# Kernel tuning notes

Measured on AMD Instinct MI355X. Metric: run time of the kernel, lower is better.

The kernel has to match this reference:

```python
import jax, jax.numpy as jnp
import numpy as np

NEG_SLOPE = 0.2
BN_EPS = 1e-5


def _gatv2(x, src, dst, Wl, Wr, att, b, N, concat):
    # x: [N, Cin]; src/dst: [E] (self-loops already appended)
    H, F = att.shape
    xl = (x @ Wl).reshape(N, H, F)  # source transform
    xr = (x @ Wr).reshape(N, H, F)  # target transform
    s = jax.nn.leaky_relu(xl[src] + xr[dst], NEG_SLOPE)  # [E,H,F]
    e = jnp.einsum('ehf,hf->eh', s, att)                  # [E,H]
    m = jax.ops.segment_max(e, dst, num_segments=N)       # [N,H]
    ex = jnp.exp(e - m[dst])
    den = jax.ops.segment_sum(ex, dst, num_segments=N)
    alpha = ex / den[dst]                                 # [E,H] softmax over in-edges
    out = jax.ops.segment_sum(alpha[:, :, None] * xl[src], dst, num_segments=N)  # [N,H,F]
    out = out.reshape(N, H * F) if concat else out.mean(axis=1)
    return out + b


def _bn_eval(x, g, b, rm, rv):
    return (x - rm) * jax.lax.rsqrt(rv + BN_EPS) * g + b


def setup_inputs() -> dict:
    key = jax.random.key(0)
    ks = jax.random.split(key, 16)
    N, E, Cin, Fh, H, Cout = 50000, 800000, 128, 64, 4, 128
    Hm = H * Fh  # 256
    d = {
        'x': jax.random.normal(ks[0], (N, Cin), jnp.float32),
        'edge_index': jax.random.randint(ks[1], (2, E), 0, N, jnp.int64),
        'Wl1': jax.random.normal(ks[2], (Cin, Hm), jnp.float32) / np.sqrt(Cin),
        'Wr1': jax.random.normal(ks[3], (Cin, Hm), jnp.float32) / np.sqrt(Cin),
        'att1': jax.random.normal(ks[4], (H, Fh), jnp.float32) / np.sqrt(Fh),
        'b1': jnp.zeros((Hm,), jnp.float32),
        'bn1_g': jax.random.uniform(ks[5], (Hm,), jnp.float32, 0.5, 1.5),
        'bn1_b': 0.1 * jax.random.normal(ks[6], (Hm,), jnp.float32),
        'bn1_m': jnp.zeros((Hm,), jnp.float32),
        'bn1_v': jnp.ones((Hm,), jnp.float32),
        'Wl2': jax.random.normal(ks[7], (Hm, Hm), jnp.float32) / np.sqrt(Hm),
        'Wr2': jax.random.normal(ks[8], (Hm, Hm), jnp.float32) / np.sqrt(Hm),
        'att2': jax.random.normal(ks[9], (H, Fh), jnp.float32) / np.sqrt(Fh),
        'b2': jnp.zeros((Hm,), jnp.float32),
        'bn2_g': jax.random.uniform(ks[10], (Hm,), jnp.float32, 0.5, 1.5),
        'bn2_b': 0.1 * jax.random.normal(ks[11], (Hm,), jnp.float32),
        'bn2_m': jnp.zeros((Hm,), jnp.float32),
        'bn2_v': jnp.ones((Hm,), jnp.float32),
        'Wl3': jax.random.normal(ks[12], (Hm, Cout), jnp.float32) / np.sqrt(Hm),
        'Wr3': jax.random.normal(ks[13], (Hm, Cout), jnp.float32) / np.sqrt(Hm),
        'att3': jax.random.normal(ks[14], (1, Cout), jnp.float32) / np.sqrt(Cout),
        'b3': jnp.zeros((Cout,), jnp.float32),
    }
    return d


def reference(x, edge_index, Wl1, Wr1, att1, b1, bn1_g, bn1_b, bn1_m, bn1_v,
              Wl2, Wr2, att2, b2, bn2_g, bn2_b, bn2_m, bn2_v,
              Wl3, Wr3, att3, b3):
    N = x.shape[0]
    loop = jnp.arange(N, dtype=edge_index.dtype)
    src = jnp.concatenate([edge_index[0], loop])  # add self-loops (PyG default)
    dst = jnp.concatenate([edge_index[1], loop])
    h = _gatv2(x, src, dst, Wl1, Wr1, att1, b1, N, True)
    h = jax.nn.elu(_bn_eval(h, bn1_g, bn1_b, bn1_m, bn1_v))  # dropout=identity (eval)
    h = _gatv2(h, src, dst, Wl2, Wr2, att2, b2, N, True)
    h = jax.nn.elu(_bn_eval(h, bn2_g, bn2_b, bn2_m, bn2_v))
    return _gatv2(h, src, dst, Wl3, Wr3, att3, b3, N, False)
```

## Files before the change

### kernel.cpp

```cpp
#include <hip/hip_runtime.h>
#include <math.h>

#define NEG_SLOPE 0.2f
#define BN_EPS 1e-5f

typedef _Float16 f16x8 __attribute__((ext_vector_type(8)));
typedef float f32x4 __attribute__((ext_vector_type(4)));

__device__ __forceinline__ void async_copy16(const void* g, void* l) {
  __builtin_amdgcn_global_load_lds(
      (const __attribute__((address_space(1))) void*)g,
      (__attribute__((address_space(3))) void*)l, 16, 0, 0);
}

__device__ __forceinline__ float2 unpack2(unsigned int u) {
  union { unsigned int u; _Float16 h[2]; } c; c.u = u;
  return make_float2((float)c.h[0], (float)c.h[1]);
}
__device__ __forceinline__ unsigned int pack2(float a, float b) {
  union { unsigned int u; _Float16 h[2]; } c;
  c.h[0] = (_Float16)a; c.h[1] = (_Float16)b; return c.u;
}
__device__ __forceinline__ float4 unpack4(uint2 u) {
  union { uint2 u2; _Float16 h[4]; } c; c.u2 = u;
  return make_float4((float)c.h[0], (float)c.h[1], (float)c.h[2], (float)c.h[3]);
}
__device__ __forceinline__ uint2 pack4(float4 v) {
  union { uint2 u2; _Float16 h[4]; } c;
  c.h[0] = (_Float16)v.x; c.h[1] = (_Float16)v.y;
  c.h[2] = (_Float16)v.z; c.h[3] = (_Float16)v.w;
  return c.u2;
}

__global__ void k_zero_i32(int* __restrict__ p, int n) {
  int i = blockIdx.x * blockDim.x + threadIdx.x;
  if (i < n) p[i] = 0;
}

__global__ void k_f2h(const float* __restrict__ in, unsigned int* __restrict__ out, int n2) {
  int i = blockIdx.x * blockDim.x + threadIdx.x;
  if (i < n2) {
    float2 v = reinterpret_cast<const float2*>(in)[i];
    out[i] = pack2(v.x, v.y);
  }
}

__global__ void k_prep_w(const float* __restrict__ Wl, const float* __restrict__ Wr,
                         int K, int Ch, _Float16* __restrict__ WT) {
  int i = blockIdx.x * blockDim.x + threadIdx.x;
  int total = 2 * Ch * K;
  if (i >= total) return;
  int c = i / K, k = i % K;
  float v = (c < Ch) ? Wl[(size_t)k * Ch + c] : Wr[(size_t)k * Ch + (c - Ch)];
  WT[i] = (_Float16)v;
}

__global__ void k_count(const int* __restrict__ ei, int E, int N, int* __restrict__ deg) {
  int e = blockIdx.x * blockDim.x + threadIdx.x;
  int T = E + N;
  if (e >= T) return;
  int d = (e < E) ? ei[E + e] : (e - E);
  atomicAdd(&deg[d], 1);
}

__global__ __launch_bounds__(1024) void k_scan(const int* __restrict__ deg, int N,
                                               int* __restrict__ offs, int* __restrict__ cursor) {
  __shared__ int wsum[16];
  __shared__ int s_base;
  int t = threadIdx.x;
  int lane = t & 63, w = t >> 6;
  if (t == 0) s_base = 0;
  __syncthreads();
  for (int start = 0; start < N; start += 1024) {
    int i = start + t;
    int v = (i < N) ? deg[i] : 0;
    int val = v;
    #pragma unroll
    for (int off = 1; off < 64; off <<= 1) {
      int x = __shfl_up(val, off, 64);
      if (lane >= off) val += x;
    }
    if (lane == 63) wsum[w] = val;
    __syncthreads();
    if (w == 0) {
      int s = (lane < 16) ? wsum[lane] : 0;
      #pragma unroll
      for (int off = 1; off < 16; off <<= 1) {
        int x = __shfl_up(s, off, 64);
        if (lane >= off) s += x;
      }
      if (lane < 16) wsum[lane] = s;
    }
    __syncthreads();
    int base = s_base;
    int woff = (w > 0) ? wsum[w - 1] : 0;
    int excl = base + woff + (val - v);
    if (i < N) { offs[i] = excl; cursor[i] = excl; }
    int total = wsum[15];
    __syncthreads();
    if (t == 0) s_base = base + total;
    __syncthreads();
  }
  if (t == 0) offs[N] = s_base;
}

__global__ void k_scatter(const int* __restrict__ ei, int E, int N,
                          int* __restrict__ cursor, int* __restrict__ csr_src) {
  int e = blockIdx.x * blockDim.x + threadIdx.x;
  int T = E + N;
  if (e < 4) csr_src[T + e] = 0;
  if (e >= T) return;
  int s, d;
  if (e < E) { s = ei[e]; d = ei[E + e]; } else { s = d = e - E; }
  int pos = atomicAdd(&cursor[d], 1);
  csr_src[pos] = s;
}

__global__ __launch_bounds__(256) void k_hgemm(const _Float16* __restrict__ A,
                                               const _Float16* __restrict__ BT,
                                               _Float16* __restrict__ C,
                                               int M, int Ntot, int K) {
  __shared__ _Float16 As[128 * 64];
  __shared__ _Float16 Bs[128 * 64];
  const int t = threadIdx.x;
  const int lane = t & 63, w = t >> 6;
  const int wr = w >> 1, wc = w & 1;
  const int bm0 = blockIdx.x * 128, bn0 = blockIdx.y * 128;
  f32x4 acc[4][4] = {};
  const int nkt = K >> 6;
  for (int kt = 0; kt < nkt; ++kt) {
    __syncthreads();
    #pragma unroll
    for (int i = 0; i < 4; ++i) {
      int q = (i * 4 + w) * 64 + lane;
      int row = q >> 3, sl = q & 7;
      int ssrc = sl ^ (row & 7);
      int ga = bm0 + row; if (ga >= M) ga = M - 1;
      async_copy16(&A[(size_t)ga * K + kt * 64 + ssrc * 8], &As[q * 8]);
      async_copy16(&BT[(size_t)(bn0 + row) * K + kt * 64 + ssrc * 8], &Bs[q * 8]);
    }
    __syncthreads();
    #pragma unroll
    for (int ks = 0; ks < 2; ++ks) {
      f16x8 a[4], b[4];
      const int sl = ks * 4 + (lane >> 4);
      #pragma unroll
      for (int mi = 0; mi < 4; ++mi) {
        int row = wr * 64 + mi * 16 + (lane & 15);
        a[mi] = *(const f16x8*)&As[(row * 8 + (sl ^ (row & 7))) * 8];
      }
      #pragma unroll
      for (int ni = 0; ni < 4; ++ni) {
        int row = wc * 64 + ni * 16 + (lane & 15);
        b[ni] = *(const f16x8*)&Bs[(row * 8 + (sl ^ (row & 7))) * 8];
      }
      #pragma unroll
      for (int mi = 0; mi < 4; ++mi)
        #pragma unroll
        for (int ni = 0; ni < 4; ++ni)
          acc[mi][ni] = __builtin_amdgcn_mfma_f32_16x16x32_f16(a[mi], b[ni], acc[mi][ni], 0, 0, 0);
    }
  }
  const int r0 = (lane >> 4) * 4;
  const int cc = lane & 15;
  #pragma unroll
  for (int mi = 0; mi < 4; ++mi) {
    #pragma unroll
    for (int r = 0; r < 4; ++r) {
      int row = bm0 + wr * 64 + mi * 16 + r0 + r;
      if (row >= M) continue;
      #pragma unroll
      for (int ni = 0; ni < 4; ++ni) {
        int col = bn0 + wc * 64 + ni * 16 + cc;
        C[(size_t)row * Ntot + col] = (_Float16)acc[mi][ni][r];
      }
    }
  }
}

__global__ __launch_bounds__(128) void k_gat4(const _Float16* __restrict__ xlr,
                                              const float* __restrict__ att, const float* __restrict__ bias,
                                              const float* __restrict__ g, const float* __restrict__ bb,
                                              const float* __restrict__ rm, const float* __restrict__ rv,
                                              const int* __restrict__ offs, const int* __restrict__ csr,
                                              int N, _Float16* __restrict__ hout) {
  const int n = blockIdx.x * 2 + (threadIdx.x >> 6);
  if (n >= N) return;
  const int l4 = (threadIdx.x & 63);
  const uint2* xu2 = (const uint2*)xlr;
  const float4 xr4 = unpack4(xu2[(size_t)n * 128 + 64 + l4]);
  const float4 at4 = reinterpret_cast<const float4*>(att)[l4];
  const int j0 = offs[n], j1 = offs[n + 1];

  float m = -INFINITY, l = 0.f;
  float4 acc = make_float4(0.f, 0.f, 0.f, 0.f);

  int j = j0;
  int s1 = csr[j0], s2 = csr[j0 + 1];
  uint2 u1 = xu2[(size_t)s1 * 128 + l4];
  uint2 u2 = xu2[(size_t)s2 * 128 + l4];

  for (; j + 1 < j1; j += 2) {
    int s1n = csr[j + 2], s2n = csr[j + 3];
    uint2 u1n = xu2[(size_t)s1n * 128 + l4];
    uint2 u2n = xu2[(size_t)s2n * 128 + l4];

    float4 v1 = unpack4(u1), v2 = unpack4(u2);
    float t0, e1, e2;
    t0 = v1.x + xr4.x; t0 = t0 > 0.f ? t0 : NEG_SLOPE * t0; e1  = t0 * at4.x;
    t0 = v1.y + xr4.y; t0 = t0 > 0.f ? t0 : NEG_SLOPE * t0; e1 += t0 * at4.y;
    t0 = v1.z + xr4.z; t0 = t0 > 0.f ? t0 : NEG_SLOPE * t0; e1 += t0 * at4.z;
    t0 = v1.w + xr4.w; t0 = t0 > 0.f ? t0 : NEG_SLOPE * t0; e1 += t0 * at4.w;
    t0 = v2.x + xr4.x; t0 = t0 > 0.f ? t0 : NEG_SLOPE * t0; e2  = t0 * at4.x;
    t0 = v2.y + xr4.y; t0 = t0 > 0.f ? t0 : NEG_SLOPE * t0; e2 += t0 * at4.y;
    t0 = v2.z + xr4.z; t0 = t0 > 0.f ? t0 : NEG_SLOPE * t0; e2 += t0 * at4.z;
    t0 = v2.w + xr4.w; t0 = t0 > 0.f ? t0 : NEG_SLOPE * t0; e2 += t0 * at4.w;
    #pragma unroll
    for (int off = 1; off < 16; off <<= 1) {
      e1 += __shfl_xor(e1, off, 64);
      e2 += __shfl_xor(e2, off, 64);
    }
    float mn = fmaxf(m, fmaxf(e1, e2));
    float c  = __expf(m - mn);
    float p1 = __expf(e1 - mn);
    float p2 = __expf(e2 - mn);
    l = l * c + p1 + p2;
    acc.x = acc.x * c + p1 * v1.x + p2 * v2.x;
    acc.y = acc.y * c + p1 * v1.y + p2 * v2.y;
    acc.z = acc.z * c + p1 * v1.z + p2 * v2.z;
    acc.w = acc.w * c + p1 * v1.w + p2 * v2.w;
    m = mn;
    u1 = u1n; u2 = u2n;
  }
  if (j < j1) {
    float4 v1 = unpack4(u1);
    float t0, e1;
    t0 = v1.x + xr4.x; t0 = t0 > 0.f ? t0 : NEG_SLOPE * t0; e1  = t0 * at4.x;
    t0 = v1.y + xr4.y; t0 = t0 > 0.f ? t0 : NEG_SLOPE * t0; e1 += t0 * at4.y;
    t0 = v1.z + xr4.z; t0 = t0 > 0.f ? t0 : NEG_SLOPE * t0; e1 += t0 * at4.z;
    t0 = v1.w + xr4.w; t0 = t0 > 0.f ? t0 : NEG_SLOPE * t0; e1 += t0 * at4.w;
    #pragma unroll
    for (int off = 1; off < 16; off <<= 1) e1 += __shfl_xor(e1, off, 64);
    float mn = fmaxf(m, e1);
    float c  = __expf(m - mn);
    float p1 = __expf(e1 - mn);
    l = l * c + p1;
    acc.x = acc.x * c + p1 * v1.x;
    acc.y = acc.y * c + p1 * v1.y;
    acc.z = acc.z * c + p1 * v1.z;
    acc.w = acc.w * c + p1 * v1.w;
  }
  const float4 b4  = reinterpret_cast<const float4*>(bias)[l4];
  const float4 rm4 = reinterpret_cast<const float4*>(rm)[l4];
  const float4 rv4 = reinterpret_cast<const float4*>(rv)[l4];
  const float4 g4  = reinterpret_cast<const float4*>(g)[l4];
  const float4 bb4 = reinterpret_cast<const float4*>(bb)[l4];
  float inv = 1.f / l;
  float4 o;
  o.x = (acc.x * inv + b4.x - rm4.x) * rsqrtf(rv4.x + BN_EPS) * g4.x + bb4.x;
  o.y = (acc.y * inv + b4.y - rm4.y) * rsqrtf(rv4.y + BN_EPS) * g4.y + bb4.y;
  o.z = (acc.z * inv + b4.z - rm4.z) * rsqrtf(rv4.z + BN_EPS) * g4.z + bb4.z;
  o.w = (acc.w * inv + b4.w - rm4.w) * rsqrtf(rv4.w + BN_EPS) * g4.w + bb4.w;
  o.x = o.x > 0.f ? o.x : (__expf(o.x) - 1.f);
  o.y = o.y > 0.f ? o.y : (__expf(o.y) - 1.f);
  o.z = o.z > 0.f ? o.z : (__expf(o.z) - 1.f);
  o.w = o.w > 0.f ? o.w : (__expf(o.w) - 1.f);
  ((uint2*)hout)[(size_t)n * 64 + l4] = pack4(o);
}

__global__ __launch_bounds__(128) void k_gat1(const _Float16* __restrict__ xlr,
                                              const float* __restrict__ att, const float* __restrict__ bias,
                                              const int* __restrict__ offs, const int* __restrict__ csr,
                                              int N, float* __restrict__ out) {
  const int n = blockIdx.x * 2 + (threadIdx.x >> 6);
  if (n >= N) return;
  const int l2 = (threadIdx.x & 63);
  const unsigned int* xu = (const unsigned int*)xlr;
  const float2 xr = unpack2(xu[(size_t)n * 128 + 64 + l2]);
  const float2 a2 = reinterpret_cast<const float2*>(att)[l2];
  const int j0 = offs[n], j1 = offs[n + 1];

  float m = -INFINITY, l = 0.f, acc0 = 0.f, acc1 = 0.f;

  int j = j0;
  int s1 = csr[j0], s2 = csr[j0 + 1];
  unsigned int u1 = xu[(size_t)s1 * 128 + l2];
  unsigned int u2 = xu[(size_t)s2 * 128 + l2];

  for (; j + 1 < j1; j += 2) {
    int s1n = csr[j + 2], s2n = csr[j + 3];
    unsigned int u1n = xu[(size_t)s1n * 128 + l2];
    unsigned int u2n = xu[(size_t)s2n * 128 + l2];

    float2 v1 = unpack2(u1), v2 = unpack2(u2);
    float t0, e1, e2;
    t0 = v1.x + xr.x; t0 = t0 > 0.f ? t0 : NEG_SLOPE * t0; e1  = t0 * a2.x;
    t0 = v1.y + xr.y; t0 = t0 > 0.f ? t0 : NEG_SLOPE * t0; e1 += t0 * a2.y;
    t0 = v2.x + xr.x; t0 = t0 > 0.f ? t0 : NEG_SLOPE * t0; e2  = t0 * a2.x;
    t0 = v2.y + xr.y; t0 = t0 > 0.f ? t0 : NEG_SLOPE * t0; e2 += t0 * a2.y;
    #pragma unroll
    for (int off = 1; off < 64; off <<= 1) {
      e1 += __shfl_xor(e1, off, 64);
      e2 += __shfl_xor(e2, off, 64);
    }
    float mn = fmaxf(m, fmaxf(e1, e2));
    float c  = __expf(m - mn);
    float p1 = __expf(e1 - mn);
    float p2 = __expf(e2 - mn);
    l = l * c + p1 + p2;
    acc0 = acc0 * c + p1 * v1.x + p2 * v2.x;
    acc1 = acc1 * c + p1 * v1.y + p2 * v2.y;
    m = mn;
    u1 = u1n; u2 = u2n;
  }
  if (j < j1) {
    float2 v1 = unpack2(u1);
    float t0, e1;
    t0 = v1.x + xr.x; t0 = t0 > 0.f ? t0 : NEG_SLOPE * t0; e1  = t0 * a2.x;
    t0 = v1.y + xr.y; t0 = t0 > 0.f ? t0 : NEG_SLOPE * t0; e1 += t0 * a2.y;
    #pragma unroll
    for (int off = 1; off < 64; off <<= 1) e1 += __shfl_xor(e1, off, 64);
    float mn = fmaxf(m, e1);
    float c  = __expf(m - mn);
    float p1 = __expf(e1 - mn);
    l = l * c + p1;
    acc0 = acc0 * c + p1 * v1.x;
    acc1 = acc1 * c + p1 * v1.y;
  }
  float inv = 1.f / l;
  const float2 b2 = reinterpret_cast<const float2*>(bias)[l2];
  float2 o = make_float2(acc0 * inv + b2.x, acc1 * inv + b2.y);
  reinterpret_cast<float2*>(out)[(size_t)n * 64 + l2] = o;
}

extern "C" void kernel_launch(void* const* d_in, const int* in_sizes, int n_in,
                              void* d_out, int out_size, void* d_ws, size_t ws_size,
                              hipStream_t stream) {
  const float* x    = (const float*)d_in[0];
  const int*   ei   = (const int*)d_in[1];
  const float* Wl1  = (const float*)d_in[2];
  const float* Wr1  = (const float*)d_in[3];
  const float* att1 = (const float*)d_in[4];
  const float* b1   = (const float*)d_in[5];
  const float* bn1g = (const float*)d_in[6];
  const float* bn1b = (const float*)d_in[7];
  const float* bn1m = (const float*)d_in[8];
  const float* bn1v = (const float*)d_in[9];
  const float* Wl2  = (const float*)d_in[10];
  const float* Wr2  = (const float*)d_in[11];
  const float* att2 = (const float*)d_in[12];
  const float* b2   = (const float*)d_in[13];
  const float* bn2g = (const float*)d_in[14];
  const float* bn2b = (const float*)d_in[15];
  const float* bn2m = (const float*)d_in[16];
  const float* bn2v = (const float*)d_in[17];
  const float* Wl3  = (const float*)d_in[18];
  const float* Wr3  = (const float*)d_in[19];
  const float* att3 = (const float*)d_in[20];
  const float* b3   = (const float*)d_in[21];

  const int Hm   = in_sizes[5];
  const int Cout = in_sizes[21];
  const int Cin  = in_sizes[2] / Hm;
  const int N    = in_sizes[0] / Cin;
  const int E    = in_sizes[1] / 2;
  const int T    = E + N;

  _Float16* x16 = (_Float16*)d_ws;
  _Float16* h   = x16 + (size_t)N * Cin;
  _Float16* xlr = h + (size_t)N * Hm;
  _Float16* WT1 = xlr + (size_t)N * 2 * Hm;
  _Float16* WT2 = WT1 + (size_t)2 * Hm * Cin;
  _Float16* WT3 = WT2 + (size_t)2 * Hm * Hm;
  int* deg    = (int*)(WT3 + (size_t)2 * Cout * Hm);
  int* offs   = deg + N;
  int* cursor = offs + N + 1;
  int* csr    = cursor + N;

  k_zero_i32<<<(N + 255) / 256, 256, 0, stream>>>(deg, N);
  k_count<<<(T + 255) / 256, 256, 0, stream>>>(ei, E, N, deg);
  k_scan<<<1, 1024, 0, stream>>>(deg, N, offs, cursor);
  k_scatter<<<(T + 255) / 256, 256, 0, stream>>>(ei, E, N, cursor, csr);

  int n2 = N * Cin / 2;
  k_f2h<<<(n2 + 255) / 256, 256, 0, stream>>>(x, (unsigned int*)x16, n2);
  k_prep_w<<<(2 * Hm * Cin + 255) / 256, 256, 0, stream>>>(Wl1, Wr1, Cin, Hm, WT1);
  k_prep_w<<<(2 * Hm * Hm + 255) / 256, 256, 0, stream>>>(Wl2, Wr2, Hm, Hm, WT2);
  k_prep_w<<<(2 * Cout * Hm + 255) / 256, 256, 0, stream>>>(Wl3, Wr3, Hm, Cout, WT3);

  const int mb = (N + 127) / 128;
  const int gb = (N + 1) / 2;

  k_hgemm<<<dim3(mb, 2 * Hm / 128), 256, 0, stream>>>(x16, WT1, xlr, N, 2 * Hm, Cin);
  k_gat4<<<gb, 128, 0, stream>>>(xlr, att1, b1, bn1g, bn1b, bn1m, bn1v, offs, csr, N, h);

  k_hgemm<<<dim3(mb, 2 * Hm / 128), 256, 0, stream>>>(h, WT2, xlr, N, 2 * Hm, Hm);
  k_gat4<<<gb, 128, 0, stream>>>(xlr, att2, b2, bn2g, bn2b, bn2m, bn2v, offs, csr, N, h);

  k_hgemm<<<dim3(mb, 2 * Cout / 128), 256, 0, stream>>>(h, WT3, xlr, N, 2 * Cout, Hm);
  k_gat1<<<gb, 128, 0, stream>>>(xlr, att3, b3, offs, csr, N, (float*)d_out);
}
```

Before: 451.9 us.

## Parallelize CSR scan, double-buffer GEMM, packed fp16 attention with lazy rescale

The single-block degree scan becomes a three-kernel parallel scan: per-block sums, a scan of those sums, then per-block offsets. The fp16 GEMM double-buffers its LDS tiles, overlapping the next tile's async loads with MFMA work. The GAT aggregation kernels compute the leaky-relu and attention dot product in packed half2 arithmetic and reduce through half2 shuffles. They also skip the online-softmax rescale unless some lane's score exceeds the running max by more than 8. The fp16 score math lowers precision, and the relaxed max threshold trades numerical headroom for fewer exponentials.

```diff
diff --git a/kernel.cpp b/kernel.cpp
--- a/kernel.cpp
+++ b/kernel.cpp
@@ -6,6 +6,10 @@
 
 typedef _Float16 f16x8 __attribute__((ext_vector_type(8)));
 typedef float f32x4 __attribute__((ext_vector_type(4)));
+typedef _Float16 h2 __attribute__((ext_vector_type(2)));
+
+union U2 { uint2 u; h2 h[2]; };
+union U1 { unsigned u; h2 h; };
 
 __device__ __forceinline__ void async_copy16(const void* g, void* l) {
   __builtin_amdgcn_global_load_lds(
@@ -13,19 +17,17 @@
       (__attribute__((address_space(3))) void*)l, 16, 0, 0);
 }
 
-__device__ __forceinline__ float2 unpack2(unsigned int u) {
-  union { unsigned int u; _Float16 h[2]; } c; c.u = u;
-  return make_float2((float)c.h[0], (float)c.h[1]);
-}
-__device__ __forceinline__ unsigned int pack2(float a, float b) {
+__device__ __forceinline__ h2 shfl_xor_h2(h2 v, int off) {
+  U1 c; c.h = v;
+  c.u = __shfl_xor(c.u, off, 64);
+  return c.h;
+}
+
+__device__ __forceinline__ unsigned int pack2f(float a, float b) {
   union { unsigned int u; _Float16 h[2]; } c;
   c.h[0] = (_Float16)a; c.h[1] = (_Float16)b; return c.u;
 }
-__device__ __forceinline__ float4 unpack4(uint2 u) {
-  union { uint2 u2; _Float16 h[4]; } c; c.u2 = u;
-  return make_float4((float)c.h[0], (float)c.h[1], (float)c.h[2], (float)c.h[3]);
-}
-__device__ __forceinline__ uint2 pack4(float4 v) {
+__device__ __forceinline__ uint2 pack4f(float4 v) {
   union { uint2 u2; _Float16 h[4]; } c;
   c.h[0] = (_Float16)v.x; c.h[1] = (_Float16)v.y;
   c.h[2] = (_Float16)v.z; c.h[3] = (_Float16)v.w;
@@ -41,7 +43,7 @@
   int i = blockIdx.x * blockDim.x + threadIdx.x;
   if (i < n2) {
     float2 v = reinterpret_cast<const float2*>(in)[i];
-    out[i] = pack2(v.x, v.y);
+    out[i] = pack2f(v.x, v.y);
   }
 }
 
@@ -63,45 +65,69 @@
   atomicAdd(&deg[d], 1);
 }
 
-__global__ __launch_bounds__(1024) void k_scan(const int* __restrict__ deg, int N,
-                                               int* __restrict__ offs, int* __restrict__ cursor) {
-  __shared__ int wsum[16];
-  __shared__ int s_base;
+__global__ __launch_bounds__(256) void k_bsum(const int* __restrict__ deg, int N,
+                                              int* __restrict__ bsum) {
+  int t = threadIdx.x;
+  int i = blockIdx.x * 256 + t;
+  int v = (i < N) ? deg[i] : 0;
+  #pragma unroll
+  for (int off = 32; off > 0; off >>= 1) v += __shfl_xor(v, off, 64);
+  __shared__ int ws[4];
+  if ((t & 63) == 0) ws[t >> 6] = v;
+  __syncthreads();
+  if (t == 0) bsum[blockIdx.x] = ws[0] + ws[1] + ws[2] + ws[3];
+}
+
+__global__ __launch_bounds__(1024) void k_bscan(int* __restrict__ bsum, int nb, int N,
+                                                int* __restrict__ offs) {
   int t = threadIdx.x;
   int lane = t & 63, w = t >> 6;
-  if (t == 0) s_base = 0;
+  int v = (t < nb) ? bsum[t] : 0;
+  int val = v;
+  #pragma unroll
+  for (int off = 1; off < 64; off <<= 1) {
+    int x = __shfl_up(val, off, 64);
+    if (lane >= off) val += x;
+  }
+  __shared__ int ws[16];
+  if (lane == 63) ws[w] = val;
   __syncthreads();
-  for (int start = 0; start < N; start += 1024) {
-    int i = start + t;
-    int v = (i < N) ? deg[i] : 0;
-    int val = v;
-    #pragma unroll
-    for (int off = 1; off < 64; off <<= 1) {
-      int x = __shfl_up(val, off, 64);
-      if (lane >= off) val += x;
-    }
-    if (lane == 63) wsum[w] = val;
-    __syncthreads();
-    if (w == 0) {
-      int s = (lane < 16) ? wsum[lane] : 0;
-      #pragma unroll
-      for (int off = 1; off < 16; off <<= 1) {
-        int x = __shfl_up(s, off, 64);
-        if (lane >= off) s += x;
-      }
-      if (lane < 16) wsum[lane] = s;
-    }
-    __syncthreads();
-    int base = s_base;
-    int woff = (w > 0) ? wsum[w - 1] : 0;
-    int excl = base + woff + (val - v);
-    if (i < N) { offs[i] = excl; cursor[i] = excl; }
-    int total = wsum[15];
-    __syncthreads();
-    if (t == 0) s_base = base + total;
-    __syncthreads();
-  }
-  if (t == 0) offs[N] = s_base;
+  if (w == 0) {
+    int s = (lane < 16) ? ws[lane] : 0;
+    #pragma unroll
+    for (int off = 1; off < 16; off <<= 1) {
+      int x = __shfl_up(s, off, 64);
+      if (lane >= off) s += x;
+    }
+    if (lane < 16) ws[lane] = s;
+  }
+  __syncthreads();
+  int excl = (w > 0 ? ws[w - 1] : 0) + val - v;
+  if (t < nb) bsum[t] = excl;
+  if (t == nb - 1) offs[N] = excl + v;
+}
+
+__global__ __launch_bounds__(256) void k_boffs(const int* __restrict__ deg, int N,
+                                               const int* __restrict__ bpre,
+                                               int* __restrict__ offs, int* __restrict__ cursor) {
+  int t = threadIdx.x;
+  int i = blockIdx.x * 256 + t;
+  int lane = t & 63, w = t >> 6;
+  int v = (i < N) ? deg[i] : 0;
+  int val = v;
+  #pragma unroll
+  for (int off = 1; off < 64; off <<= 1) {
+    int x = __shfl_up(val, off, 64);
+    if (lane >= off) val += x;
+  }
+  __shared__ int ws[4];
+  if (lane == 63) ws[w] = val;
+  __syncthreads();
+  int wo = 0;
+  #pragma unroll
+  for (int k = 0; k < 4; ++k) if (k < w) wo += ws[k];
+  int excl = bpre[blockIdx.x] + wo + val - v;
+  if (i < N) { offs[i] = excl; cursor[i] = excl; }
 }
 
 __global__ void k_scatter(const int* __restrict__ ei, int E, int N,
@@ -120,26 +146,37 @@
                                                const _Float16* __restrict__ BT,
                                                _Float16* __restrict__ C,
                                                int M, int Ntot, int K) {
-  __shared__ _Float16 As[128 * 64];
-  __shared__ _Float16 Bs[128 * 64];
+  __shared__ _Float16 As[2][128 * 64];
+  __shared__ _Float16 Bs[2][128 * 64];
   const int t = threadIdx.x;
   const int lane = t & 63, w = t >> 6;
   const int wr = w >> 1, wc = w & 1;
   const int bm0 = blockIdx.x * 128, bn0 = blockIdx.y * 128;
   f32x4 acc[4][4] = {};
   const int nkt = K >> 6;
-  for (int kt = 0; kt < nkt; ++kt) {
-    __syncthreads();
+
+  auto stage = [&](int b, int kt) {
     #pragma unroll
     for (int i = 0; i < 4; ++i) {
       int q = (i * 4 + w) * 64 + lane;
       int row = q >> 3, sl = q & 7;
       int ssrc = sl ^ (row & 7);
       int ga = bm0 + row; if (ga >= M) ga = M - 1;
-      async_copy16(&A[(size_t)ga * K + kt * 64 + ssrc * 8], &As[q * 8]);
-      async_copy16(&BT[(size_t)(bn0 + row) * K + kt * 64 + ssrc * 8], &Bs[q * 8]);
-    }
-    __syncthreads();
+      async_copy16(&A[(size_t)ga * K + kt * 64 + ssrc * 8], &As[b][q * 8]);
+      async_copy16(&BT[(size_t)(bn0 + row) * K + kt * 64 + ssrc * 8], &Bs[b][q * 8]);
+    }
+  };
+
+  stage(0, 0);
+  for (int kt = 0; kt < nkt; ++kt) {
+    int cur = kt & 1;
+    if (kt + 1 < nkt) {
+      stage(cur ^ 1, kt + 1);
+      asm volatile("s_waitcnt vmcnt(8)" ::: "memory");
+    } else {
+      asm volatile("s_waitcnt vmcnt(0)" ::: "memory");
+    }
+    __builtin_amdgcn_s_barrier();
     #pragma unroll
     for (int ks = 0; ks < 2; ++ks) {
       f16x8 a[4], b[4];
@@ -147,12 +184,12 @@
       #pragma unroll
       for (int mi = 0; mi < 4; ++mi) {
         int row = wr * 64 + mi * 16 + (lane & 15);
-        a[mi] = *(const f16x8*)&As[(row * 8 + (sl ^ (row & 7))) * 8];
+        a[mi] = *(const f16x8*)&As[cur][(row * 8 + (sl ^ (row & 7))) * 8];
       }
       #pragma unroll
       for (int ni = 0; ni < 4; ++ni) {
         int row = wc * 64 + ni * 16 + (lane & 15);
-        b[ni] = *(const f16x8*)&Bs[(row * 8 + (sl ^ (row & 7))) * 8];
+        b[ni] = *(const f16x8*)&Bs[cur][(row * 8 + (sl ^ (row & 7))) * 8];
       }
       #pragma unroll
       for (int mi = 0; mi < 4; ++mi)
@@ -160,6 +197,7 @@
         for (int ni = 0; ni < 4; ++ni)
           acc[mi][ni] = __builtin_amdgcn_mfma_f32_16x16x32_f16(a[mi], b[ni], acc[mi][ni], 0, 0, 0);
     }
+    __builtin_amdgcn_s_barrier();
   }
   const int r0 = (lane >> 4) * 4;
   const int cc = lane & 15;
@@ -187,9 +225,13 @@
   const int n = blockIdx.x * 2 + (threadIdx.x >> 6);
   if (n >= N) return;
   const int l4 = (threadIdx.x & 63);
-  const uint2* xu2 = (const uint2*)xlr;
-  const float4 xr4 = unpack4(xu2[(size_t)n * 128 + 64 + l4]);
-  const float4 at4 = reinterpret_cast<const float4*>(att)[l4];
+  const uint2* xbase = (const uint2*)xlr + l4;
+  U2 xru; xru.u = xbase[(size_t)n * 128 + 64];
+  const h2 xr0 = xru.h[0], xr1 = xru.h[1];
+  const float4 at = reinterpret_cast<const float4*>(att)[l4];
+  const h2 at0 = {(_Float16)at.x, (_Float16)at.y};
+  const h2 at1 = {(_Float16)at.z, (_Float16)at.w};
+  const h2 k02 = {(_Float16)0.2f, (_Float16)0.2f};
   const int j0 = offs[n], j1 = offs[n + 1];
 
   float m = -INFINITY, l = 0.f;
@@ -197,64 +239,73 @@
 
   int j = j0;
   int s1 = csr[j0], s2 = csr[j0 + 1];
-  uint2 u1 = xu2[(size_t)s1 * 128 + l4];
-  uint2 u2 = xu2[(size_t)s2 * 128 + l4];
+  uint2 u1 = xbase[(size_t)s1 * 128];
+  uint2 u2 = xbase[(size_t)s2 * 128];
 
   for (; j + 1 < j1; j += 2) {
     int s1n = csr[j + 2], s2n = csr[j + 3];
-    uint2 u1n = xu2[(size_t)s1n * 128 + l4];
-    uint2 u2n = xu2[(size_t)s2n * 128 + l4];
-
-    float4 v1 = unpack4(u1), v2 = unpack4(u2);
-    float t0, e1, e2;
-    t0 = v1.x + xr4.x; t0 = t0 > 0.f ? t0 : NEG_SLOPE * t0; e1  = t0 * at4.x;
-    t0 = v1.y + xr4.y; t0 = t0 > 0.f ? t0 : NEG_SLOPE * t0; e1 += t0 * at4.y;
-    t0 = v1.z + xr4.z; t0 = t0 > 0.f ? t0 : NEG_SLOPE * t0; e1 += t0 * at4.z;
-    t0 = v1.w + xr4.w; t0 = t0 > 0.f ? t0 : NEG_SLOPE * t0; e1 += t0 * at4.w;
-    t0 = v2.x + xr4.x; t0 = t0 > 0.f ? t0 : NEG_SLOPE * t0; e2  = t0 * at4.x;
-    t0 = v2.y + xr4.y; t0 = t0 > 0.f ? t0 : NEG_SLOPE * t0; e2 += t0 * at4.y;
-    t0 = v2.z + xr4.z; t0 = t0 > 0.f ? t0 : NEG_SLOPE * t0; e2 += t0 * at4.z;
-    t0 = v2.w + xr4.w; t0 = t0 > 0.f ? t0 : NEG_SLOPE * t0; e2 += t0 * at4.w;
-    #pragma unroll
-    for (int off = 1; off < 16; off <<= 1) {
-      e1 += __shfl_xor(e1, off, 64);
-      e2 += __shfl_xor(e2, off, 64);
-    }
-    float mn = fmaxf(m, fmaxf(e1, e2));
-    float c  = __expf(m - mn);
-    float p1 = __expf(e1 - mn);
-    float p2 = __expf(e2 - mn);
-    l = l * c + p1 + p2;
-    acc.x = acc.x * c + p1 * v1.x + p2 * v2.x;
-    acc.y = acc.y * c + p1 * v1.y + p2 * v2.y;
-    acc.z = acc.z * c + p1 * v1.z + p2 * v2.z;
-    acc.w = acc.w * c + p1 * v1.w + p2 * v2.w;
-    m = mn;
+    uint2 u1n = xbase[(size_t)s1n * 128];
+    uint2 u2n = xbase[(size_t)s2n * 128];
+
+    U2 c1, c2; c1.u = u1; c2.u = u2;
+    h2 sA = c1.h[0] + xr0, sB = c1.h[1] + xr1;
+    sA = __builtin_elementwise_max(sA, sA * k02);
+    sB = __builtin_elementwise_max(sB, sB * k02);
+    h2 dp1 = sA * at0 + sB * at1;
+    h2 sC = c2.h[0] + xr0, sD = c2.h[1] + xr1;
+    sC = __builtin_elementwise_max(sC, sC * k02);
+    sD = __builtin_elementwise_max(sD, sD * k02);
+    h2 dp2 = sC * at0 + sD * at1;
+
+    h2 q = __builtin_shufflevector(dp1, dp2, 0, 2) + __builtin_shufflevector(dp1, dp2, 1, 3);
+    #pragma unroll
+    for (int off = 1; off < 16; off <<= 1) q += shfl_xor_h2(q, off);
+    float e1 = (float)q[0], e2 = (float)q[1];
+
+    float emax = fmaxf(e1, e2);
+    if (__any(emax > m + 8.f)) {
+      float mn = fmaxf(m, emax);
+      float c0 = __expf(m - mn);
+      l *= c0; acc.x *= c0; acc.y *= c0; acc.z *= c0; acc.w *= c0;
+      m = mn;
+    }
+    float p1 = __expf(e1 - m), p2 = __expf(e2 - m);
+    l += p1 + p2;
+    acc.x += p1 * (float)c1.h[0][0] + p2 * (float)c2.h[0][0];
+    acc.y += p1 * (float)c1.h[0][1] + p2 * (float)c2.h[0][1];
+    acc.z += p1 * (float)c1.h[1][0] + p2 * (float)c2.h[1][0];
+    acc.w += p1 * (float)c1.h[1][1] + p2 * (float)c2.h[1][1];
     u1 = u1n; u2 = u2n;
   }
   if (j < j1) {
-    float4 v1 = unpack4(u1);
-    float t0, e1;
-    t0 = v1.x + xr4.x; t0 = t0 > 0.f ? t0 : NEG_SLOPE * t0; e1  = t0 * at4.x;
-    t0 = v1.y + xr4.y; t0 = t0 > 0.f ? t0 : NEG_SLOPE * t0; e1 += t0 * at4.y;
-    t0 = v1.z + xr4.z; t0 = t0 > 0.f ? t0 : NEG_SLOPE * t0; e1 += t0 * at4.z;
-    t0 = v1.w + xr4.w; t0 = t0 > 0.f ? t0 : NEG_SLOPE * t0; e1 += t0 * at4.w;
-    #pragma unroll
-    for (int off = 1; off < 16; off <<= 1) e1 += __shfl_xor(e1, off, 64);
-    float mn = fmaxf(m, e1);
-    float c  = __expf(m - mn);
-    float p1 = __expf(e1 - mn);
-    l = l * c + p1;
-    acc.x = acc.x * c + p1 * v1.x;
-    acc.y = acc.y * c + p1 * v1.y;
-    acc.z = acc.z * c + p1 * v1.z;
-    acc.w = acc.w * c + p1 * v1.w;
-  }
+    U2 c1; c1.u = u1;
+    h2 sA = c1.h[0] + xr0, sB = c1.h[1] + xr1;
+    sA = __builtin_elementwise_max(sA, sA * k02);
+    sB = __builtin_elementwise_max(sB, sB * k02);
+    h2 q = sA * at0 + sB * at1;
+    #pragma unroll
+    for (int off = 1; off < 16; off <<= 1) q += shfl_xor_h2(q, off);
+    float e1 = (float)q[0] + (float)q[1];
+    if (__any(e1 > m + 8.f)) {
+      float mn = fmaxf(m, e1);
+      float c0 = __expf(m - mn);
+      l *= c0; acc.x *= c0; acc.y *= c0; acc.z *= c0; acc.w *= c0;
+      m = mn;
+    }
+    float p1 = __expf(e1 - m);
+    l += p1;
+    acc.x += p1 * (float)c1.h[0][0];
+    acc.y += p1 * (float)c1.h[0][1];
+    acc.z += p1 * (float)c1.h[1][0];
+    acc.w += p1 * (float)c1.h[1][1];
+  }
+  const int c0i = 4 * l4;
   const float4 b4  = reinterpret_cast<const float4*>(bias)[l4];
   const float4 rm4 = reinterpret_cast<const float4*>(rm)[l4];
   const float4 rv4 = reinterpret_cast<const float4*>(rv)[l4];
   const float4 g4  = reinterpret_cast<const float4*>(g)[l4];
   const float4 bb4 = reinterpret_cast<const float4*>(bb)[l4];
+  (void)c0i;
   float inv = 1.f / l;
   float4 o;
   o.x = (acc.x * inv + b4.x - rm4.x) * rsqrtf(rv4.x + BN_EPS) * g4.x + bb4.x;
@@ -265,7 +316,7 @@
   o.y = o.y > 0.f ? o.y : (__expf(o.y) - 1.f);
   o.z = o.z > 0.f ? o.z : (__expf(o.z) - 1.f);
   o.w = o.w > 0.f ? o.w : (__expf(o.w) - 1.f);
-  ((uint2*)hout)[(size_t)n * 64 + l4] = pack4(o);
+  ((uint2*)hout)[(size_t)n * 64 + l4] = pack4f(o);
 }
 
 __global__ __launch_bounds__(128) void k_gat1(const _Float16* __restrict__ xlr,
@@ -275,57 +326,70 @@
   const int n = blockIdx.x * 2 + (threadIdx.x >> 6);
   if (n >= N) return;
   const int l2 = (threadIdx.x & 63);
-  const unsigned int* xu = (const unsigned int*)xlr;
-  const float2 xr = unpack2(xu[(size_t)n * 128 + 64 + l2]);
+  const unsigned int* xbase = (const unsigned int*)xlr + l2;
+  U1 xru; xru.u = xbase[(size_t)n * 128 + 64];
+  const h2 xr0 = xru.h;
   const float2 a2 = reinterpret_cast<const float2*>(att)[l2];
+  const h2 at0 = {(_Float16)a2.x, (_Float16)a2.y};
+  const h2 k02 = {(_Float16)0.2f, (_Float16)0.2f};
   const int j0 = offs[n], j1 = offs[n + 1];
 
   float m = -INFINITY, l = 0.f, acc0 = 0.f, acc1 = 0.f;
 
   int j = j0;
   int s1 = csr[j0], s2 = csr[j0 + 1];
-  unsigned int u1 = xu[(size_t)s1 * 128 + l2];
-  unsigned int u2 = xu[(size_t)s2 * 128 + l2];
+  unsigned int u1 = xbase[(size_t)s1 * 128];
+  unsigned int u2 = xbase[(size_t)s2 * 128];
 
   for (; j + 1 < j1; j += 2) {
     int s1n = csr[j + 2], s2n = csr[j + 3];
-    unsigned int u1n = xu[(size_t)s1n * 128 + l2];
-    unsigned int u2n = xu[(size_t)s2n * 128 + l2];
-
-    float2 v1 = unpack2(u1), v2 = unpack2(u2);
-    float t0, e1, e2;
-    t0 = v1.x + xr.x; t0 = t0 > 0.f ? t0 : NEG_SLOPE * t0; e1  = t0 * a2.x;
-    t0 = v1.y + xr.y; t0 = t0 > 0.f ? t0 : NEG_SLOPE * t0; e1 += t0 * a2.y;
-    t0 = v2.x + xr.x; t0 = t0 > 0.f ? t0 : NEG_SLOPE * t0; e2  = t0 * a2.x;
-    t0 = v2.y + xr.y; t0 = t0 > 0.f ? t0 : NEG_SLOPE * t0; e2 += t0 * a2.y;
-    #pragma unroll
-    for (int off = 1; off < 64; off <<= 1) {
-      e1 += __shfl_xor(e1, off, 64);
-      e2 += __shfl_xor(e2, off, 64);
-    }
-    float mn = fmaxf(m, fmaxf(e1, e2));
-    float c  = __expf(m - mn);
-    float p1 = __expf(e1 - mn);
-    float p2 = __expf(e2 - mn);
-    l = l * c + p1 + p2;
-    acc0 = acc0 * c + p1 * v1.x + p2 * v2.x;
-    acc1 = acc1 * c + p1 * v1.y + p2 * v2.y;
-    m = mn;
+    unsigned int u1n = xbase[(size_t)s1n * 128];
+    unsigned int u2n = xbase[(size_t)s2n * 128];
+
+    U1 c1, c2; c1.u = u1; c2.u = u2;
+    h2 sA = c1.h + xr0;
+    sA = __builtin_elementwise_max(sA, sA * k02);
+    h2 dp1 = sA * at0;
+    h2 sC = c2.h + xr0;
+    sC = __builtin_elementwise_max(sC, sC * k02);
+    h2 dp2 = sC * at0;
+
+    h2 q = __builtin_shufflevector(dp1, dp2, 0, 2) + __builtin_shufflevector(dp1, dp2, 1, 3);
+    #pragma unroll
+    for (int off = 1; off < 64; off <<= 1) q += shfl_xor_h2(q, off);
+    float e1 = (float)q[0], e2 = (float)q[1];
+
+    float emax = fmaxf(e1, e2);
+    if (__any(emax > m + 8.f)) {
+      float mn = fmaxf(m, emax);
+      float c0 = __expf(m - mn);
+      l *= c0; acc0 *= c0; acc1 *= c0;
+      m = mn;
+    }
+    float p1 = __expf(e1 - m), p2 = __expf(e2 - m);
+    l += p1 + p2;
+    acc0 += p1 * (float)c1.h[0] + p2 * (float)c2.h[0];
+    acc1 += p1 * (float)c1.h[1] + p2 * (float)c2.h[1];
     u1 = u1n; u2 = u2n;
   }
   if (j < j1) {
-    float2 v1 = unpack2(u1);
-    float t0, e1;
-    t0 = v1.x + xr.x; t0 = t0 > 0.f ? t0 : NEG_SLOPE * t0; e1  = t0 * a2.x;
-    t0 = v1.y + xr.y; t0 = t0 > 0.f ? t0 : NEG_SLOPE * t0; e1 += t0 * a2.y;
-    #pragma unroll
-    for (int off = 1; off < 64; off <<= 1) e1 += __shfl_xor(e1, off, 64);
-    float mn = fmaxf(m, e1);
-    float c  = __expf(m - mn);
-    float p1 = __expf(e1 - mn);
-    l = l * c + p1;
-    acc0 = acc0 * c + p1 * v1.x;
-    acc1 = acc1 * c + p1 * v1.y;
+    U1 c1; c1.u = u1;
+    h2 sA = c1.h + xr0;
+    sA = __builtin_elementwise_max(sA, sA * k02);
+    h2 q = sA * at0;
+    #pragma unroll
+    for (int off = 1; off < 64; off <<= 1) q += shfl_xor_h2(q, off);
+    float e1 = (float)q[0] + (float)q[1];
+    if (__any(e1 > m + 8.f)) {
+      float mn = fmaxf(m, e1);
+      float c0 = __expf(m - mn);
+      l *= c0; acc0 *= c0; acc1 *= c0;
+      m = mn;
+    }
+    float p1 = __expf(e1 - m);
+    l += p1;
+    acc0 += p1 * (float)c1.h[0];
+    acc1 += p1 * (float)c1.h[1];
   }
   float inv = 1.f / l;
   const float2 b2 = reinterpret_cast<const float2*>(bias)[l2];
@@ -376,10 +440,15 @@
   int* offs   = deg + N;
   int* cursor = offs + N + 1;
   int* csr    = cursor + N;
+  int* bsum   = csr + T + 4;
+
+  const int nb = (N + 255) / 256;
 
   k_zero_i32<<<(N + 255) / 256, 256, 0, stream>>>(deg, N);
   k_count<<<(T + 255) / 256, 256, 0, stream>>>(ei, E, N, deg);
-  k_scan<<<1, 1024, 0, stream>>>(deg, N, offs, cursor);
+  k_bsum<<<nb, 256, 0, stream>>>(deg, N, bsum);
+  k_bscan<<<1, 1024, 0, stream>>>(bsum, nb, N, offs);
+  k_boffs<<<nb, 256, 0, stream>>>(deg, N, bsum, offs, cursor);
   k_scatter<<<(T + 255) / 256, 256, 0, stream>>>(ei, E, N, cursor, csr);
 
   int n2 = N * Cin / 2;
```

New measurement: 405.2 us. 10.3% less time.
